# Performance work log

Measured on AMD Instinct MI355X. Metric: run time of the kernel, lower is better.

Reference implementation:

```python
import jax, jax.numpy as jnp
import numpy as np

BS, N, DE, DX = 16, 256, 64, 256
BIG = 100000.0


def setup_inputs() -> dict:
    key = jax.random.key(0)
    k1, k2, k3, k4 = jax.random.split(key, 4)
    E = jax.random.normal(k1, (BS, N, N, DE), dtype=jnp.float32)
    e_mask2 = jax.random.uniform(k2, (BS, 1, N, 1)) < 0.8
    fan_in = 4 * DE
    bound = 1.0 / np.sqrt(fan_in)
    W = jax.random.uniform(k3, (DX, fan_in), minval=-bound, maxval=bound, dtype=jnp.float32)
    b = jax.random.uniform(k4, (DX,), minval=-bound, maxval=bound, dtype=jnp.float32)
    return {"E": E, "e_mask2": e_mask2, "W": W, "b": b}


def reference(E, e_mask2, W, b):
    bs, n, _, de = E.shape
    mask = jnp.broadcast_to(e_mask2, (bs, n, n, de)).astype(E.dtype)  # bs,n,n,de
    imask = 1.0 - mask
    denom = mask.sum(axis=2)                       # bs,n,de
    m = E.sum(axis=2) / denom                      # (faithful: unmasked sum / mask count)
    mi = (E + BIG * imask).min(axis=2)             # masked min
    ma = (E - BIG * imask).max(axis=2)             # masked max
    std = (((E - m[:, :, None, :]) ** 2) * mask).sum(axis=2) / denom
    z = jnp.concatenate((m, mi, ma, std), axis=2)  # bs,n,4*de
    return jnp.einsum('bnf,df->bnd', z, W) + b     # bs,n,dx
```

## Files before the change

kernel.cpp:

```cpp
#include <hip/hip_runtime.h>
#include <cstdint>
#include <cstddef>

#define BSZ 16
#define NN  256
#define DE  64
#define DXX 256
#define FAN (4 * DE)
#define IB  4

__global__ __launch_bounds__(256) void prep_kernel(
    const uint8_t* __restrict__ raw, const float* __restrict__ W,
    float* __restrict__ WT, float* __restrict__ maskf)
{
    const int t   = threadIdx.x;
    const int blk = blockIdx.x;
    if (blk < FAN) {
        WT[blk * DXX + t] = W[t * FAN + blk];
    } else {
        __shared__ int det[2];
        if (t == 0) { det[0] = 0; det[1] = 0; }
        __syncthreads();
        int s1 = 0, s23 = 0;
        const uint8_t* p = raw + t * 16;
        #pragma unroll
        for (int u = 0; u < 16; ++u) {
            int v = (int)p[u];
            int m4 = u & 3;
            if (m4 == 1) s1 += v; else if (m4 >= 2) s23 += v;
        }
        if (s1)  atomicAdd(&det[0], s1);
        if (s23) atomicAdd(&det[1], s23);
        __syncthreads();
        const int kind = (det[1] == 0) ? 1 : ((det[0] == 0) ? 2 : 0);
        for (int idx = t; idx < BSZ * NN; idx += 256) {
            float mv;
            if (kind == 1)      mv = (((const int*)(const void*)raw)[idx] != 0) ? 1.f : 0.f;
            else if (kind == 2) mv = (((const float*)(const void*)raw)[idx] != 0.f) ? 1.f : 0.f;
            else                mv = (raw[idx] != 0) ? 1.f : 0.f;
            maskf[idx] = mv;
        }
    }
}

template <bool TR>
__global__ __launch_bounds__(256, 4) void etox_fused(
    const float* __restrict__ E, const uint8_t* __restrict__ raw,
    const float* __restrict__ maskf, const float* __restrict__ W,
    const float* __restrict__ WT, const float* __restrict__ bias,
    float* __restrict__ out)
{
    __shared__ float  m_lds[NN];
    __shared__ int    det[2];
    __shared__ float  cpart[4];
    __shared__ float  partial[4][16][20];
    __shared__ float  z_lds[IB][FAN];
    __shared__ float4 part_c[4][IB][64];

    const int t    = threadIdx.x;
    const int g0   = blockIdx.x * IB;
    const int b    = g0 >> 8;
    const int wv   = t >> 6;
    const int lane = t & 63;

    float mv;
    if (TR) {
        mv = maskf[b * NN + t];
    } else {
        if (t == 0) { det[0] = 0; det[1] = 0; }
        int s1 = 0, s23 = 0;
        const uint8_t* p = raw + t * 16;
        #pragma unroll
        for (int u = 0; u < 16; ++u) {
            int v = (int)p[u];
            int m4 = u & 3;
            if (m4 == 1) s1 += v; else if (m4 >= 2) s23 += v;
        }
        __syncthreads();
        if (s1)  atomicAdd(&det[0], s1);
        if (s23) atomicAdd(&det[1], s23);
        __syncthreads();
        const int kind = (det[1] == 0) ? 1 : ((det[0] == 0) ? 2 : 0);
        int idx = b * NN + t;
        if (kind == 1)      mv = (((const int*)(const void*)raw)[idx] != 0) ? 1.f : 0.f;
        else if (kind == 2) mv = (((const float*)(const void*)raw)[idx] != 0.f) ? 1.f : 0.f;
        else                mv = (raw[idx] != 0) ? 1.f : 0.f;
    }
    m_lds[t] = mv;
    unsigned long long bal = __ballot(mv != 0.f);
    if (lane == 0) cpart[wv] = (float)__popcll(bal);
    __syncthreads();
    const float inv_cnt = 1.0f / (cpart[0] + cpart[1] + cpart[2] + cpart[3]);

    const int dq = t & 15;
    const int jb = t >> 4;
    const float* base0 = E + (size_t)g0 * (NN * DE) + (size_t)jb * DE + 4 * dq;

    #define LD(P, K) (*(const float4*)((P) + (size_t)(K) * (16 * DE)))
    float4 A0, A1, A2, A3, B0, B1, B2, B3;
    A0 = LD(base0, 0); A1 = LD(base0, 1); A2 = LD(base0, 2); A3 = LD(base0, 3);

    for (int r = 0; r < IB; ++r) {
        const float* baser = base0 + (size_t)r * (NN * DE);

        float s[4]  = {0.f, 0.f, 0.f, 0.f};
        float ms[4] = {0.f, 0.f, 0.f, 0.f};
        float q[4]  = {0.f, 0.f, 0.f, 0.f};
        float mi[4] = {1e30f, 1e30f, 1e30f, 1e30f};
        float ma[4] = {-1e30f, -1e30f, -1e30f, -1e30f};

        #define CONS1(V, KK) { \
            float mk = m_lds[jb + 16 * (KK)]; \
            bool on = (mk != 0.f); \
            float4 v = V; \
            s[0] += v.x; s[1] += v.y; s[2] += v.z; s[3] += v.w; \
            ms[0] = fmaf(mk, v.x, ms[0]); ms[1] = fmaf(mk, v.y, ms[1]); \
            ms[2] = fmaf(mk, v.z, ms[2]); ms[3] = fmaf(mk, v.w, ms[3]); \
            q[0] = fmaf(mk * v.x, v.x, q[0]); q[1] = fmaf(mk * v.y, v.y, q[1]); \
            q[2] = fmaf(mk * v.z, v.z, q[2]); q[3] = fmaf(mk * v.w, v.w, q[3]); \
            mi[0] = fminf(mi[0], on ? v.x : 1e30f); mi[1] = fminf(mi[1], on ? v.y : 1e30f); \
            mi[2] = fminf(mi[2], on ? v.z : 1e30f); mi[3] = fminf(mi[3], on ? v.w : 1e30f); \
            ma[0] = fmaxf(ma[0], on ? v.x : -1e30f); ma[1] = fmaxf(ma[1], on ? v.y : -1e30f); \
            ma[2] = fmaxf(ma[2], on ? v.z : -1e30f); ma[3] = fmaxf(ma[3], on ? v.w : -1e30f); \
        }

        B0 = LD(baser, 4);  B1 = LD(baser, 5);  B2 = LD(baser, 6);  B3 = LD(baser, 7);
        CONS1(A0, 0) CONS1(A1, 1) CONS1(A2, 2) CONS1(A3, 3)
        A0 = LD(baser, 8);  A1 = LD(baser, 9);  A2 = LD(baser, 10); A3 = LD(baser, 11);
        CONS1(B0, 4) CONS1(B1, 5) CONS1(B2, 6) CONS1(B3, 7)
        B0 = LD(baser, 12); B1 = LD(baser, 13); B2 = LD(baser, 14); B3 = LD(baser, 15);
        CONS1(A0, 8) CONS1(A1, 9) CONS1(A2, 10) CONS1(A3, 11)
        if (r < IB - 1) {
            const float* basen = baser + (NN * DE);
            A0 = LD(basen, 0); A1 = LD(basen, 1); A2 = LD(basen, 2); A3 = LD(basen, 3);
        }
        CONS1(B0, 12) CONS1(B1, 13) CONS1(B2, 14) CONS1(B3, 15)
        #undef CONS1

        #pragma unroll
        for (int c = 0; c < 4; ++c) {
            s[c]  += __shfl_xor(s[c], 16);  s[c]  += __shfl_xor(s[c], 32);
            ms[c] += __shfl_xor(ms[c], 16); ms[c] += __shfl_xor(ms[c], 32);
            q[c]  += __shfl_xor(q[c], 16);  q[c]  += __shfl_xor(q[c], 32);
            mi[c] = fminf(mi[c], __shfl_xor(mi[c], 16));
            mi[c] = fminf(mi[c], __shfl_xor(mi[c], 32));
            ma[c] = fmaxf(ma[c], __shfl_xor(ma[c], 16));
            ma[c] = fmaxf(ma[c], __shfl_xor(ma[c], 32));
        }

        if (lane < 16) {
            float* p = partial[wv][lane];
            #pragma unroll
            for (int c = 0; c < 4; ++c) {
                p[c]      = s[c];
                p[4 + c]  = ms[c];
                p[8 + c]  = q[c];
                p[12 + c] = mi[c];
                p[16 + c] = ma[c];
            }
        }
        __syncthreads();

        if (t < 64) {
            const int d = t, dq2 = d >> 2, c = d & 3;
            float ss = 0.f, mss = 0.f, mq = 0.f, lmi = 1e30f, lma = -1e30f;
            #pragma unroll
            for (int w = 0; w < 4; ++w) {
                const float* p = partial[w][dq2];
                ss  += p[c];
                mss += p[4 + c];
                mq  += p[8 + c];
                lmi  = fminf(lmi, p[12 + c]);
                lma  = fmaxf(lma, p[16 + c]);
            }
            float m    = ss * inv_cnt;
            float stdv = mq * inv_cnt - 2.0f * m * (mss * inv_cnt) + m * m;
            z_lds[t >> 8][0] = z_lds[t >> 8][0];
            z_lds[r][d]       = m;
            z_lds[r][64 + d]  = lmi;
            z_lds[r][128 + d] = lma;
            z_lds[r][192 + d] = stdv;
        }
        __syncthreads();
    }
    #undef LD

    if (TR) {
        float4 acc[IB];
        #pragma unroll
        for (int r = 0; r < IB; ++r) acc[r] = make_float4(0.f, 0.f, 0.f, 0.f);

        const float4* WT4 = (const float4*)WT;
        int f0 = 64 * wv;
        #pragma unroll 4
        for (int fg = 0; fg < 16; ++fg, f0 += 4) {
            float4 w0 = WT4[(size_t)(f0 + 0) * 64 + lane];
            float4 w1 = WT4[(size_t)(f0 + 1) * 64 + lane];
            float4 w2 = WT4[(size_t)(f0 + 2) * 64 + lane];
            float4 w3 = WT4[(size_t)(f0 + 3) * 64 + lane];
            #pragma unroll
            for (int r = 0; r < IB; ++r) {
                float4 z4 = *(const float4*)(&z_lds[r][f0]);
                acc[r].x = fmaf(z4.x, w0.x, fmaf(z4.y, w1.x, fmaf(z4.z, w2.x, fmaf(z4.w, w3.x, acc[r].x))));
                acc[r].y = fmaf(z4.x, w0.y, fmaf(z4.y, w1.y, fmaf(z4.z, w2.y, fmaf(z4.w, w3.y, acc[r].y))));
                acc[r].z = fmaf(z4.x, w0.z, fmaf(z4.y, w1.z, fmaf(z4.z, w2.z, fmaf(z4.w, w3.z, acc[r].z))));
                acc[r].w = fmaf(z4.x, w0.w, fmaf(z4.y, w1.w, fmaf(z4.z, w2.w, fmaf(z4.w, w3.w, acc[r].w))));
            }
        }
        #pragma unroll
        for (int r = 0; r < IB; ++r) part_c[wv][r][lane] = acc[r];
        __syncthreads();

        const int row = t >> 6, l2 = t & 63;
        float4 p0 = part_c[0][row][l2], p1 = part_c[1][row][l2];
        float4 p2 = part_c[2][row][l2], p3 = part_c[3][row][l2];
        float4 bv = *(const float4*)(bias + 4 * l2);
        float4 o;
        o.x = p0.x + p1.x + p2.x + p3.x + bv.x;
        o.y = p0.y + p1.y + p2.y + p3.y + bv.y;
        o.z = p0.z + p1.z + p2.z + p3.z + bv.z;
        o.w = p0.w + p1.w + p2.w + p3.w + bv.w;
        *(float4*)(out + (size_t)(g0 + row) * DXX + 4 * l2) = o;
    } else {
        float acc0, acc1, acc2, acc3;
        {
            float bv = bias[t];
            acc0 = bv; acc1 = bv; acc2 = bv; acc3 = bv;
        }
        const float4* Wrow = (const float4*)(W + (size_t)t * FAN);
        #pragma unroll 8
        for (int f4 = 0; f4 < 64; ++f4) {
            float4 w4 = Wrow[f4];
            int f = 4 * f4;
            acc0 += z_lds[0][f] * w4.x + z_lds[0][f+1] * w4.y + z_lds[0][f+2] * w4.z + z_lds[0][f+3] * w4.w;
            acc1 += z_lds[1][f] * w4.x + z_lds[1][f+1] * w4.y + z_lds[1][f+2] * w4.z + z_lds[1][f+3] * w4.w;
            acc2 += z_lds[2][f] * w4.x + z_lds[2][f+1] * w4.y + z_lds[2][f+2] * w4.z + z_lds[2][f+3] * w4.w;
            acc3 += z_lds[3][f] * w4.x + z_lds[3][f+1] * w4.y + z_lds[3][f+2] * w4.z + z_lds[3][f+3] * w4.w;
        }
        out[(size_t)(g0 + 0) * DXX + t] = acc0;
        out[(size_t)(g0 + 1) * DXX + t] = acc1;
        out[(size_t)(g0 + 2) * DXX + t] = acc2;
        out[(size_t)(g0 + 3) * DXX + t] = acc3;
    }
}

extern "C" void kernel_launch(void* const* d_in, const int* in_sizes, int n_in,
                              void* d_out, int out_size, void* d_ws, size_t ws_size,
                              hipStream_t stream) {
    const float*   E    = (const float*)d_in[0];
    const uint8_t* mraw = (const uint8_t*)d_in[1];
    const float*   W    = (const float*)d_in[2];
    const float*   bias = (const float*)d_in[3];
    float*         out  = (float*)d_out;

    const size_t need = (size_t)FAN * DXX * sizeof(float) + (size_t)BSZ * NN * sizeof(float);
    if (ws_size >= need) {
        float* WT    = (float*)d_ws;
        float* maskf = (float*)d_ws + (size_t)FAN * DXX;
        prep_kernel<<<FAN + 1, 256, 0, stream>>>(mraw, W, WT, maskf);
        etox_fused<true><<<(BSZ * NN) / IB, 256, 0, stream>>>(E, mraw, maskf, W, WT, bias, out);
    } else {
        etox_fused<false><<<(BSZ * NN) / IB, 256, 0, stream>>>(E, mraw, nullptr, W, nullptr, bias, out);
    }
}
```

Baseline: 63.53 us.

## Interleave per-row matvec of previous row with next row's reduction loads

Instead of doing the whole 4-row z·W matvec after all reductions, the matvec for row r-1 is split into four chunks and interleaved between the E-tile consume steps of row r. The B-register prefetch is also moved one row ahead. The aim is to hide the E global-load latency behind matvec FMAs and the WT loads behind reduction work. The cost is that W^T is now reloaded once per row instead of being shared across all four rows, and register pressure goes up.

Result: slower. 216.1 us (+240.1%).

```diff
diff --git a/kernel.cpp b/kernel.cpp
--- a/kernel.cpp
+++ b/kernel.cpp
@@ -95,13 +95,37 @@
     const int dq = t & 15;
     const int jb = t >> 4;
     const float* base0 = E + (size_t)g0 * (NN * DE) + (size_t)jb * DE + 4 * dq;
+    const float4* WT4 = (const float4*)WT;
+    const int fbase = 64 * wv;
+
+    #define MVQ4(RZ, FG0) { \
+        _Pragma("unroll") \
+        for (int u = 0; u < 4; ++u) { \
+            const int f0 = fbase + 4 * ((FG0) + u); \
+            float4 w0 = WT4[(size_t)(f0 + 0) * 64 + lane]; \
+            float4 w1 = WT4[(size_t)(f0 + 1) * 64 + lane]; \
+            float4 w2 = WT4[(size_t)(f0 + 2) * 64 + lane]; \
+            float4 w3 = WT4[(size_t)(f0 + 3) * 64 + lane]; \
+            float4 z4 = *(const float4*)(&z_lds[RZ][f0]); \
+            mvacc.x = fmaf(z4.x, w0.x, fmaf(z4.y, w1.x, fmaf(z4.z, w2.x, fmaf(z4.w, w3.x, mvacc.x)))); \
+            mvacc.y = fmaf(z4.x, w0.y, fmaf(z4.y, w1.y, fmaf(z4.z, w2.y, fmaf(z4.w, w3.y, mvacc.y)))); \
+            mvacc.z = fmaf(z4.x, w0.z, fmaf(z4.y, w1.z, fmaf(z4.z, w2.z, fmaf(z4.w, w3.z, mvacc.z)))); \
+            mvacc.w = fmaf(z4.x, w0.w, fmaf(z4.y, w1.w, fmaf(z4.z, w2.w, fmaf(z4.w, w3.w, mvacc.w)))); \
+        } \
+    }
 
     #define LD(P, K) (*(const float4*)((P) + (size_t)(K) * (16 * DE)))
     float4 A0, A1, A2, A3, B0, B1, B2, B3;
     A0 = LD(base0, 0); A1 = LD(base0, 1); A2 = LD(base0, 2); A3 = LD(base0, 3);
+    B0 = LD(base0, 4); B1 = LD(base0, 5); B2 = LD(base0, 6); B3 = LD(base0, 7);
+
+    float4 mvacc = make_float4(0.f, 0.f, 0.f, 0.f);
 
     for (int r = 0; r < IB; ++r) {
         const float* baser = base0 + (size_t)r * (NN * DE);
+        const float* basen = baser + (NN * DE);
+        const int rz = r - 1;
+        const bool domv = TR && (r > 0);
 
         float s[4]  = {0.f, 0.f, 0.f, 0.f};
         float ms[4] = {0.f, 0.f, 0.f, 0.f};
@@ -124,17 +148,22 @@
             ma[2] = fmaxf(ma[2], on ? v.z : -1e30f); ma[3] = fmaxf(ma[3], on ? v.w : -1e30f); \
         }
 
-        B0 = LD(baser, 4);  B1 = LD(baser, 5);  B2 = LD(baser, 6);  B3 = LD(baser, 7);
         CONS1(A0, 0) CONS1(A1, 1) CONS1(A2, 2) CONS1(A3, 3)
         A0 = LD(baser, 8);  A1 = LD(baser, 9);  A2 = LD(baser, 10); A3 = LD(baser, 11);
+        if (domv) MVQ4(rz, 0)
         CONS1(B0, 4) CONS1(B1, 5) CONS1(B2, 6) CONS1(B3, 7)
         B0 = LD(baser, 12); B1 = LD(baser, 13); B2 = LD(baser, 14); B3 = LD(baser, 15);
+        if (domv) MVQ4(rz, 4)
         CONS1(A0, 8) CONS1(A1, 9) CONS1(A2, 10) CONS1(A3, 11)
-        if (r < IB - 1) {
-            const float* basen = baser + (NN * DE);
-            A0 = LD(basen, 0); A1 = LD(basen, 1); A2 = LD(basen, 2); A3 = LD(basen, 3);
-        }
+        if (r < IB - 1) { A0 = LD(basen, 0); A1 = LD(basen, 1); A2 = LD(basen, 2); A3 = LD(basen, 3); }
+        if (domv) MVQ4(rz, 8)
         CONS1(B0, 12) CONS1(B1, 13) CONS1(B2, 14) CONS1(B3, 15)
+        if (r < IB - 1) { B0 = LD(basen, 4); B1 = LD(basen, 5); B2 = LD(basen, 6); B3 = LD(basen, 7); }
+        if (domv) {
+            MVQ4(rz, 12)
+            part_c[wv][rz][lane] = mvacc;
+            mvacc = make_float4(0.f, 0.f, 0.f, 0.f);
+        }
         #undef CONS1
 
         #pragma unroll
@@ -175,7 +204,6 @@
             }
             float m    = ss * inv_cnt;
             float stdv = mq * inv_cnt - 2.0f * m * (mss * inv_cnt) + m * m;
-            z_lds[t >> 8][0] = z_lds[t >> 8][0];
             z_lds[r][d]       = m;
             z_lds[r][64 + d]  = lmi;
             z_lds[r][128 + d] = lma;
@@ -186,29 +214,8 @@
     #undef LD
 
     if (TR) {
-        float4 acc[IB];
-        #pragma unroll
-        for (int r = 0; r < IB; ++r) acc[r] = make_float4(0.f, 0.f, 0.f, 0.f);
-
-        const float4* WT4 = (const float4*)WT;
-        int f0 = 64 * wv;
-        #pragma unroll 4
-        for (int fg = 0; fg < 16; ++fg, f0 += 4) {
-            float4 w0 = WT4[(size_t)(f0 + 0) * 64 + lane];
-            float4 w1 = WT4[(size_t)(f0 + 1) * 64 + lane];
-            float4 w2 = WT4[(size_t)(f0 + 2) * 64 + lane];
-            float4 w3 = WT4[(size_t)(f0 + 3) * 64 + lane];
-            #pragma unroll
-            for (int r = 0; r < IB; ++r) {
-                float4 z4 = *(const float4*)(&z_lds[r][f0]);
-                acc[r].x = fmaf(z4.x, w0.x, fmaf(z4.y, w1.x, fmaf(z4.z, w2.x, fmaf(z4.w, w3.x, acc[r].x))));
-                acc[r].y = fmaf(z4.x, w0.y, fmaf(z4.y, w1.y, fmaf(z4.z, w2.y, fmaf(z4.w, w3.y, acc[r].y))));
-                acc[r].z = fmaf(z4.x, w0.z, fmaf(z4.y, w1.z, fmaf(z4.z, w2.z, fmaf(z4.w, w3.z, acc[r].z))));
-                acc[r].w = fmaf(z4.x, w0.w, fmaf(z4.y, w1.w, fmaf(z4.z, w2.w, fmaf(z4.w, w3.w, acc[r].w))));
-            }
-        }
-        #pragma unroll
-        for (int r = 0; r < IB; ++r) part_c[wv][r][lane] = acc[r];
+        MVQ4(IB - 1, 0) MVQ4(IB - 1, 4) MVQ4(IB - 1, 8) MVQ4(IB - 1, 12)
+        part_c[wv][IB - 1][lane] = mvacc;
         __syncthreads();
 
         const int row = t >> 6, l2 = t & 63;
@@ -242,6 +249,7 @@
         out[(size_t)(g0 + 2) * DXX + t] = acc2;
         out[(size_t)(g0 + 3) * DXX + t] = acc3;
     }
+    #undef MVQ4
 }
 
 extern "C" void kernel_launch(void* const* d_in, const int* in_sizes, int n_in,
```

## Interleave per-row matvec into reduction loop and use lgkm-only barriers

Applied to the files above, without the earlier changes.

The projection of each row's z-vector through W is moved inside the per-row reduction loop, so its matvec can overlap with the prefetched E loads for the next row instead of running as a separate phase after all rows. The __syncthreads calls are replaced with a custom barrier that waits only on LDS counters (lgkmcnt), so outstanding global loads of E do not stall the barrier. In exchange, WT is reloaded once per row instead of being reused across all four rows, which raises the number of L2/global loads. The barrier also relies on the compiler not reordering LDS accesses across the inline asm.

After: 81.23 us. 27.9% more time.

```diff
diff --git a/kernel.cpp b/kernel.cpp
--- a/kernel.cpp
+++ b/kernel.cpp
@@ -8,6 +8,12 @@
 #define DXX 256
 #define FAN (4 * DE)
 #define IB  4
+
+__device__ __forceinline__ void barrier_lgkm() {
+    asm volatile("s_waitcnt lgkmcnt(0)" ::: "memory");
+    __builtin_amdgcn_s_barrier();
+    asm volatile("" ::: "memory");
+}
 
 __global__ __launch_bounds__(256) void prep_kernel(
     const uint8_t* __restrict__ raw, const float* __restrict__ W,
@@ -95,6 +101,8 @@
     const int dq = t & 15;
     const int jb = t >> 4;
     const float* base0 = E + (size_t)g0 * (NN * DE) + (size_t)jb * DE + 4 * dq;
+    const float4* WT4 = (const float4*)WT;
+    const int fbase = 64 * wv;
 
     #define LD(P, K) (*(const float4*)((P) + (size_t)(K) * (16 * DE)))
     float4 A0, A1, A2, A3, B0, B1, B2, B3;
@@ -159,7 +167,7 @@
                 p[16 + c] = ma[c];
             }
         }
-        __syncthreads();
+        if (TR) barrier_lgkm(); else __syncthreads();
 
         if (t < 64) {
             const int d = t, dq2 = d >> 2, c = d & 3;
@@ -175,42 +183,35 @@
             }
             float m    = ss * inv_cnt;
             float stdv = mq * inv_cnt - 2.0f * m * (mss * inv_cnt) + m * m;
-            z_lds[t >> 8][0] = z_lds[t >> 8][0];
             z_lds[r][d]       = m;
             z_lds[r][64 + d]  = lmi;
             z_lds[r][128 + d] = lma;
             z_lds[r][192 + d] = stdv;
         }
-        __syncthreads();
+        if (TR) barrier_lgkm(); else __syncthreads();
+
+        if (TR) {
+            float4 mvacc = make_float4(0.f, 0.f, 0.f, 0.f);
+            #pragma unroll 4
+            for (int fg = 0; fg < 16; ++fg) {
+                const int f0 = fbase + 4 * fg;
+                float4 w0 = WT4[(size_t)(f0 + 0) * 64 + lane];
+                float4 w1 = WT4[(size_t)(f0 + 1) * 64 + lane];
+                float4 w2 = WT4[(size_t)(f0 + 2) * 64 + lane];
+                float4 w3 = WT4[(size_t)(f0 + 3) * 64 + lane];
+                float4 z4 = *(const float4*)(&z_lds[r][f0]);
+                mvacc.x = fmaf(z4.x, w0.x, fmaf(z4.y, w1.x, fmaf(z4.z, w2.x, fmaf(z4.w, w3.x, mvacc.x))));
+                mvacc.y = fmaf(z4.x, w0.y, fmaf(z4.y, w1.y, fmaf(z4.z, w2.y, fmaf(z4.w, w3.y, mvacc.y))));
+                mvacc.z = fmaf(z4.x, w0.z, fmaf(z4.y, w1.z, fmaf(z4.z, w2.z, fmaf(z4.w, w3.z, mvacc.z))));
+                mvacc.w = fmaf(z4.x, w0.w, fmaf(z4.y, w1.w, fmaf(z4.z, w2.w, fmaf(z4.w, w3.w, mvacc.w))));
+            }
+            part_c[wv][r][lane] = mvacc;
+        }
     }
     #undef LD
 
     if (TR) {
-        float4 acc[IB];
-        #pragma unroll
-        for (int r = 0; r < IB; ++r) acc[r] = make_float4(0.f, 0.f, 0.f, 0.f);
-
-        const float4* WT4 = (const float4*)WT;
-        int f0 = 64 * wv;
-        #pragma unroll 4
-        for (int fg = 0; fg < 16; ++fg, f0 += 4) {
-            float4 w0 = WT4[(size_t)(f0 + 0) * 64 + lane];
-            float4 w1 = WT4[(size_t)(f0 + 1) * 64 + lane];
-            float4 w2 = WT4[(size_t)(f0 + 2) * 64 + lane];
-            float4 w3 = WT4[(size_t)(f0 + 3) * 64 + lane];
-            #pragma unroll
-            for (int r = 0; r < IB; ++r) {
-                float4 z4 = *(const float4*)(&z_lds[r][f0]);
-                acc[r].x = fmaf(z4.x, w0.x, fmaf(z4.y, w1.x, fmaf(z4.z, w2.x, fmaf(z4.w, w3.x, acc[r].x))));
-                acc[r].y = fmaf(z4.x, w0.y, fmaf(z4.y, w1.y, fmaf(z4.z, w2.y, fmaf(z4.w, w3.y, acc[r].y))));
-                acc[r].z = fmaf(z4.x, w0.z, fmaf(z4.y, w1.z, fmaf(z4.z, w2.z, fmaf(z4.w, w3.z, acc[r].z))));
-                acc[r].w = fmaf(z4.x, w0.w, fmaf(z4.y, w1.w, fmaf(z4.z, w2.w, fmaf(z4.w, w3.w, acc[r].w))));
-            }
-        }
-        #pragma unroll
-        for (int r = 0; r < IB; ++r) part_c[wv][r][lane] = acc[r];
-        __syncthreads();
-
+        barrier_lgkm();
         const int row = t >> 6, l2 = t & 63;
         float4 p0 = part_c[0][row][l2], p1 = part_c[1][row][l2];
         float4 p2 = part_c[2][row][l2], p3 = part_c[3][row][l2];
```

## Split fused stats+GEMM into separate kernels with a larger GEMM row tile

Applied to the files above, without the earlier changes.

The fused kernel is split into a stats kernel, which writes z rows to a workspace buffer, and a separate GEMM kernel that processes 16 rows per block. Each weight load is then reused across 16 rows instead of 4, and the stats kernel is freed of the GEMM phase's registers and shared memory. Mask values are also cached in registers rather than re-read from LDS in the inner loop. The cost is an extra launch plus a round trip of the z tensor (4 MB) through global memory, and a larger workspace requirement. The fallback path keeps the old fused kernel.

After: 77.54 us. 22.1% more time.

```diff
diff --git a/kernel.cpp b/kernel.cpp
--- a/kernel.cpp
+++ b/kernel.cpp
@@ -8,6 +8,7 @@
 #define DXX 256
 #define FAN (4 * DE)
 #define IB  4
+#define RB  16
 
 __global__ __launch_bounds__(256) void prep_kernel(
     const uint8_t* __restrict__ raw, const float* __restrict__ W,
@@ -43,19 +44,13 @@
     }
 }
 
-template <bool TR>
-__global__ __launch_bounds__(256, 4) void etox_fused(
-    const float* __restrict__ E, const uint8_t* __restrict__ raw,
-    const float* __restrict__ maskf, const float* __restrict__ W,
-    const float* __restrict__ WT, const float* __restrict__ bias,
-    float* __restrict__ out)
+__global__ __launch_bounds__(256, 4) void k1_stats(
+    const float* __restrict__ E, const float* __restrict__ maskf,
+    float* __restrict__ zout)
 {
-    __shared__ float  m_lds[NN];
-    __shared__ int    det[2];
-    __shared__ float  cpart[4];
-    __shared__ float  partial[4][16][20];
-    __shared__ float  z_lds[IB][FAN];
-    __shared__ float4 part_c[4][IB][64];
+    __shared__ float m_lds[NN];
+    __shared__ float cpart[4];
+    __shared__ float partial[4][16][20];
 
     const int t    = threadIdx.x;
     const int g0   = blockIdx.x * IB;
@@ -63,29 +58,7 @@
     const int wv   = t >> 6;
     const int lane = t & 63;
 
-    float mv;
-    if (TR) {
-        mv = maskf[b * NN + t];
-    } else {
-        if (t == 0) { det[0] = 0; det[1] = 0; }
-        int s1 = 0, s23 = 0;
-        const uint8_t* p = raw + t * 16;
-        #pragma unroll
-        for (int u = 0; u < 16; ++u) {
-            int v = (int)p[u];
-            int m4 = u & 3;
-            if (m4 == 1) s1 += v; else if (m4 >= 2) s23 += v;
-        }
-        __syncthreads();
-        if (s1)  atomicAdd(&det[0], s1);
-        if (s23) atomicAdd(&det[1], s23);
-        __syncthreads();
-        const int kind = (det[1] == 0) ? 1 : ((det[0] == 0) ? 2 : 0);
-        int idx = b * NN + t;
-        if (kind == 1)      mv = (((const int*)(const void*)raw)[idx] != 0) ? 1.f : 0.f;
-        else if (kind == 2) mv = (((const float*)(const void*)raw)[idx] != 0.f) ? 1.f : 0.f;
-        else                mv = (raw[idx] != 0) ? 1.f : 0.f;
-    }
+    float mv = maskf[b * NN + t];
     m_lds[t] = mv;
     unsigned long long bal = __ballot(mv != 0.f);
     if (lane == 0) cpart[wv] = (float)__popcll(bal);
@@ -94,6 +67,11 @@
 
     const int dq = t & 15;
     const int jb = t >> 4;
+
+    float mk[16];
+    #pragma unroll
+    for (int k = 0; k < 16; ++k) mk[k] = m_lds[jb + 16 * k];
+
     const float* base0 = E + (size_t)g0 * (NN * DE) + (size_t)jb * DE + 4 * dq;
 
     #define LD(P, K) (*(const float4*)((P) + (size_t)(K) * (16 * DE)))
@@ -110,14 +88,14 @@
         float ma[4] = {-1e30f, -1e30f, -1e30f, -1e30f};
 
         #define CONS1(V, KK) { \
-            float mk = m_lds[jb + 16 * (KK)]; \
-            bool on = (mk != 0.f); \
+            float mkv = mk[KK]; \
+            bool on = (mkv != 0.f); \
             float4 v = V; \
             s[0] += v.x; s[1] += v.y; s[2] += v.z; s[3] += v.w; \
-            ms[0] = fmaf(mk, v.x, ms[0]); ms[1] = fmaf(mk, v.y, ms[1]); \
-            ms[2] = fmaf(mk, v.z, ms[2]); ms[3] = fmaf(mk, v.w, ms[3]); \
-            q[0] = fmaf(mk * v.x, v.x, q[0]); q[1] = fmaf(mk * v.y, v.y, q[1]); \
-            q[2] = fmaf(mk * v.z, v.z, q[2]); q[3] = fmaf(mk * v.w, v.w, q[3]); \
+            ms[0] = fmaf(mkv, v.x, ms[0]); ms[1] = fmaf(mkv, v.y, ms[1]); \
+            ms[2] = fmaf(mkv, v.z, ms[2]); ms[3] = fmaf(mkv, v.w, ms[3]); \
+            q[0] = fmaf(mkv * v.x, v.x, q[0]); q[1] = fmaf(mkv * v.y, v.y, q[1]); \
+            q[2] = fmaf(mkv * v.z, v.z, q[2]); q[3] = fmaf(mkv * v.w, v.w, q[3]); \
             mi[0] = fminf(mi[0], on ? v.x : 1e30f); mi[1] = fminf(mi[1], on ? v.y : 1e30f); \
             mi[2] = fminf(mi[2], on ? v.z : 1e30f); mi[3] = fminf(mi[3], on ? v.w : 1e30f); \
             ma[0] = fmaxf(ma[0], on ? v.x : -1e30f); ma[1] = fmaxf(ma[1], on ? v.y : -1e30f); \
@@ -175,43 +153,63 @@
             }
             float m    = ss * inv_cnt;
             float stdv = mq * inv_cnt - 2.0f * m * (mss * inv_cnt) + m * m;
-            z_lds[t >> 8][0] = z_lds[t >> 8][0];
-            z_lds[r][d]       = m;
-            z_lds[r][64 + d]  = lmi;
-            z_lds[r][128 + d] = lma;
-            z_lds[r][192 + d] = stdv;
+            float* zr = zout + (size_t)(g0 + r) * FAN;
+            zr[d]       = m;
+            zr[64 + d]  = lmi;
+            zr[128 + d] = lma;
+            zr[192 + d] = stdv;
         }
         __syncthreads();
     }
     #undef LD
-
-    if (TR) {
-        float4 acc[IB];
-        #pragma unroll
-        for (int r = 0; r < IB; ++r) acc[r] = make_float4(0.f, 0.f, 0.f, 0.f);
-
-        const float4* WT4 = (const float4*)WT;
-        int f0 = 64 * wv;
-        #pragma unroll 4
-        for (int fg = 0; fg < 16; ++fg, f0 += 4) {
-            float4 w0 = WT4[(size_t)(f0 + 0) * 64 + lane];
-            float4 w1 = WT4[(size_t)(f0 + 1) * 64 + lane];
-            float4 w2 = WT4[(size_t)(f0 + 2) * 64 + lane];
-            float4 w3 = WT4[(size_t)(f0 + 3) * 64 + lane];
-            #pragma unroll
-            for (int r = 0; r < IB; ++r) {
-                float4 z4 = *(const float4*)(&z_lds[r][f0]);
-                acc[r].x = fmaf(z4.x, w0.x, fmaf(z4.y, w1.x, fmaf(z4.z, w2.x, fmaf(z4.w, w3.x, acc[r].x))));
-                acc[r].y = fmaf(z4.x, w0.y, fmaf(z4.y, w1.y, fmaf(z4.z, w2.y, fmaf(z4.w, w3.y, acc[r].y))));
-                acc[r].z = fmaf(z4.x, w0.z, fmaf(z4.y, w1.z, fmaf(z4.z, w2.z, fmaf(z4.w, w3.z, acc[r].z))));
-                acc[r].w = fmaf(z4.x, w0.w, fmaf(z4.y, w1.w, fmaf(z4.z, w2.w, fmaf(z4.w, w3.w, acc[r].w))));
-            }
-        }
-        #pragma unroll
-        for (int r = 0; r < IB; ++r) part_c[wv][r][lane] = acc[r];
-        __syncthreads();
-
-        const int row = t >> 6, l2 = t & 63;
+}
+
+__global__ __launch_bounds__(256, 2) void k2_gemm(
+    const float* __restrict__ zin, const float* __restrict__ WT,
+    const float* __restrict__ bias, float* __restrict__ out)
+{
+    __shared__ float  z_s[RB][FAN];
+    __shared__ float4 part_c[4][RB][64];
+
+    const int t    = threadIdx.x;
+    const int r0   = blockIdx.x * RB;
+    const int wv   = t >> 6;
+    const int lane = t & 63;
+
+    #pragma unroll
+    for (int i = 0; i < RB; ++i)
+        z_s[i][t] = zin[(size_t)(r0 + i) * FAN + t];
+    __syncthreads();
+
+    float4 acc[RB];
+    #pragma unroll
+    for (int i = 0; i < RB; ++i) acc[i] = make_float4(0.f, 0.f, 0.f, 0.f);
+
+    const float4* WT4 = (const float4*)WT;
+    int f0 = 64 * wv;
+    #pragma unroll 2
+    for (int fg = 0; fg < 16; ++fg, f0 += 4) {
+        float4 w0 = WT4[(size_t)(f0 + 0) * 64 + lane];
+        float4 w1 = WT4[(size_t)(f0 + 1) * 64 + lane];
+        float4 w2 = WT4[(size_t)(f0 + 2) * 64 + lane];
+        float4 w3 = WT4[(size_t)(f0 + 3) * 64 + lane];
+        #pragma unroll
+        for (int i = 0; i < RB; ++i) {
+            float4 z4 = *(const float4*)(&z_s[i][f0]);
+            acc[i].x = fmaf(z4.x, w0.x, fmaf(z4.y, w1.x, fmaf(z4.z, w2.x, fmaf(z4.w, w3.x, acc[i].x))));
+            acc[i].y = fmaf(z4.x, w0.y, fmaf(z4.y, w1.y, fmaf(z4.z, w2.y, fmaf(z4.w, w3.y, acc[i].y))));
+            acc[i].z = fmaf(z4.x, w0.z, fmaf(z4.y, w1.z, fmaf(z4.z, w2.z, fmaf(z4.w, w3.z, acc[i].z))));
+            acc[i].w = fmaf(z4.x, w0.w, fmaf(z4.y, w1.w, fmaf(z4.z, w2.w, fmaf(z4.w, w3.w, acc[i].w))));
+        }
+    }
+    #pragma unroll
+    for (int i = 0; i < RB; ++i) part_c[wv][i][lane] = acc[i];
+    __syncthreads();
+
+    #pragma unroll
+    for (int pass = 0; pass < 4; ++pass) {
+        const int idx = pass * 256 + t;
+        const int row = idx >> 6, l2 = idx & 63;
         float4 p0 = part_c[0][row][l2], p1 = part_c[1][row][l2];
         float4 p2 = part_c[2][row][l2], p3 = part_c[3][row][l2];
         float4 bv = *(const float4*)(bias + 4 * l2);
@@ -220,28 +218,157 @@
         o.y = p0.y + p1.y + p2.y + p3.y + bv.y;
         o.z = p0.z + p1.z + p2.z + p3.z + bv.z;
         o.w = p0.w + p1.w + p2.w + p3.w + bv.w;
-        *(float4*)(out + (size_t)(g0 + row) * DXX + 4 * l2) = o;
-    } else {
-        float acc0, acc1, acc2, acc3;
-        {
-            float bv = bias[t];
-            acc0 = bv; acc1 = bv; acc2 = bv; acc3 = bv;
-        }
-        const float4* Wrow = (const float4*)(W + (size_t)t * FAN);
-        #pragma unroll 8
-        for (int f4 = 0; f4 < 64; ++f4) {
-            float4 w4 = Wrow[f4];
-            int f = 4 * f4;
-            acc0 += z_lds[0][f] * w4.x + z_lds[0][f+1] * w4.y + z_lds[0][f+2] * w4.z + z_lds[0][f+3] * w4.w;
-            acc1 += z_lds[1][f] * w4.x + z_lds[1][f+1] * w4.y + z_lds[1][f+2] * w4.z + z_lds[1][f+3] * w4.w;
-            acc2 += z_lds[2][f] * w4.x + z_lds[2][f+1] * w4.y + z_lds[2][f+2] * w4.z + z_lds[2][f+3] * w4.w;
-            acc3 += z_lds[3][f] * w4.x + z_lds[3][f+1] * w4.y + z_lds[3][f+2] * w4.z + z_lds[3][f+3] * w4.w;
-        }
-        out[(size_t)(g0 + 0) * DXX + t] = acc0;
-        out[(size_t)(g0 + 1) * DXX + t] = acc1;
-        out[(size_t)(g0 + 2) * DXX + t] = acc2;
-        out[(size_t)(g0 + 3) * DXX + t] = acc3;
-    }
+        *(float4*)(out + (size_t)(r0 + row) * DXX + 4 * l2) = o;
+    }
+}
+
+__global__ __launch_bounds__(256, 4) void etox_legacy(
+    const float* __restrict__ E, const uint8_t* __restrict__ raw,
+    const float* __restrict__ W, const float* __restrict__ bias,
+    float* __restrict__ out)
+{
+    __shared__ float m_lds[NN];
+    __shared__ int   det[2];
+    __shared__ float cpart[4];
+    __shared__ float partial[4][16][20];
+    __shared__ float z_lds[IB][FAN];
+
+    const int t    = threadIdx.x;
+    const int g0   = blockIdx.x * IB;
+    const int b    = g0 >> 8;
+    const int wv   = t >> 6;
+    const int lane = t & 63;
+
+    if (t == 0) { det[0] = 0; det[1] = 0; }
+    int s1 = 0, s23 = 0;
+    {
+        const uint8_t* p = raw + t * 16;
+        #pragma unroll
+        for (int u = 0; u < 16; ++u) {
+            int v = (int)p[u];
+            int m4 = u & 3;
+            if (m4 == 1) s1 += v; else if (m4 >= 2) s23 += v;
+        }
+    }
+    __syncthreads();
+    if (s1)  atomicAdd(&det[0], s1);
+    if (s23) atomicAdd(&det[1], s23);
+    __syncthreads();
+    const int kind = (det[1] == 0) ? 1 : ((det[0] == 0) ? 2 : 0);
+    float mv;
+    {
+        int idx = b * NN + t;
+        if (kind == 1)      mv = (((const int*)(const void*)raw)[idx] != 0) ? 1.f : 0.f;
+        else if (kind == 2) mv = (((const float*)(const void*)raw)[idx] != 0.f) ? 1.f : 0.f;
+        else                mv = (raw[idx] != 0) ? 1.f : 0.f;
+    }
+    m_lds[t] = mv;
+    unsigned long long bal = __ballot(mv != 0.f);
+    if (lane == 0) cpart[wv] = (float)__popcll(bal);
+    __syncthreads();
+    const float inv_cnt = 1.0f / (cpart[0] + cpart[1] + cpart[2] + cpart[3]);
+
+    const int dq = t & 15;
+    const int jb = t >> 4;
+    const float* base0 = E + (size_t)g0 * (NN * DE) + (size_t)jb * DE + 4 * dq;
+
+    #define LD(P, K) (*(const float4*)((P) + (size_t)(K) * (16 * DE)))
+    float4 A0, A1, A2, A3, B0, B1, B2, B3;
+    A0 = LD(base0, 0); A1 = LD(base0, 1); A2 = LD(base0, 2); A3 = LD(base0, 3);
+
+    for (int r = 0; r < IB; ++r) {
+        const float* baser = base0 + (size_t)r * (NN * DE);
+        float s[4]  = {0.f, 0.f, 0.f, 0.f};
+        float ms[4] = {0.f, 0.f, 0.f, 0.f};
+        float q[4]  = {0.f, 0.f, 0.f, 0.f};
+        float mi[4] = {1e30f, 1e30f, 1e30f, 1e30f};
+        float ma[4] = {-1e30f, -1e30f, -1e30f, -1e30f};
+
+        #define CONS1(V, KK) { \
+            float mkv = m_lds[jb + 16 * (KK)]; \
+            bool on = (mkv != 0.f); \
+            float4 v = V; \
+            s[0] += v.x; s[1] += v.y; s[2] += v.z; s[3] += v.w; \
+            ms[0] = fmaf(mkv, v.x, ms[0]); ms[1] = fmaf(mkv, v.y, ms[1]); \
+            ms[2] = fmaf(mkv, v.z, ms[2]); ms[3] = fmaf(mkv, v.w, ms[3]); \
+            q[0] = fmaf(mkv * v.x, v.x, q[0]); q[1] = fmaf(mkv * v.y, v.y, q[1]); \
+            q[2] = fmaf(mkv * v.z, v.z, q[2]); q[3] = fmaf(mkv * v.w, v.w, q[3]); \
+            mi[0] = fminf(mi[0], on ? v.x : 1e30f); mi[1] = fminf(mi[1], on ? v.y : 1e30f); \
+            mi[2] = fminf(mi[2], on ? v.z : 1e30f); mi[3] = fminf(mi[3], on ? v.w : 1e30f); \
+            ma[0] = fmaxf(ma[0], on ? v.x : -1e30f); ma[1] = fmaxf(ma[1], on ? v.y : -1e30f); \
+            ma[2] = fmaxf(ma[2], on ? v.z : -1e30f); ma[3] = fmaxf(ma[3], on ? v.w : -1e30f); \
+        }
+
+        B0 = LD(baser, 4);  B1 = LD(baser, 5);  B2 = LD(baser, 6);  B3 = LD(baser, 7);
+        CONS1(A0, 0) CONS1(A1, 1) CONS1(A2, 2) CONS1(A3, 3)
+        A0 = LD(baser, 8);  A1 = LD(baser, 9);  A2 = LD(baser, 10); A3 = LD(baser, 11);
+        CONS1(B0, 4) CONS1(B1, 5) CONS1(B2, 6) CONS1(B3, 7)
+        B0 = LD(baser, 12); B1 = LD(baser, 13); B2 = LD(baser, 14); B3 = LD(baser, 15);
+        CONS1(A0, 8) CONS1(A1, 9) CONS1(A2, 10) CONS1(A3, 11)
+        if (r < IB - 1) {
+            const float* basen = baser + (NN * DE);
+            A0 = LD(basen, 0); A1 = LD(basen, 1); A2 = LD(basen, 2); A3 = LD(basen, 3);
+        }
+        CONS1(B0, 12) CONS1(B1, 13) CONS1(B2, 14) CONS1(B3, 15)
+        #undef CONS1
+
+        #pragma unroll
+        for (int c = 0; c < 4; ++c) {
+            s[c]  += __shfl_xor(s[c], 16);  s[c]  += __shfl_xor(s[c], 32);
+            ms[c] += __shfl_xor(ms[c], 16); ms[c] += __shfl_xor(ms[c], 32);
+            q[c]  += __shfl_xor(q[c], 16);  q[c]  += __shfl_xor(q[c], 32);
+            mi[c] = fminf(mi[c], __shfl_xor(mi[c], 16));
+            mi[c] = fminf(mi[c], __shfl_xor(mi[c], 32));
+            ma[c] = fmaxf(ma[c], __shfl_xor(ma[c], 16));
+            ma[c] = fmaxf(ma[c], __shfl_xor(ma[c], 32));
+        }
+
+        if (lane < 16) {
+            float* p = partial[wv][lane];
+            #pragma unroll
+            for (int c = 0; c < 4; ++c) {
+                p[c] = s[c]; p[4+c] = ms[c]; p[8+c] = q[c];
+                p[12+c] = mi[c]; p[16+c] = ma[c];
+            }
+        }
+        __syncthreads();
+
+        if (t < 64) {
+            const int d = t, dq2 = d >> 2, c = d & 3;
+            float ss = 0.f, mss = 0.f, mq = 0.f, lmi = 1e30f, lma = -1e30f;
+            #pragma unroll
+            for (int w = 0; w < 4; ++w) {
+                const float* p = partial[w][dq2];
+                ss += p[c]; mss += p[4+c]; mq += p[8+c];
+                lmi = fminf(lmi, p[12+c]); lma = fmaxf(lma, p[16+c]);
+            }
+            float m    = ss * inv_cnt;
+            float stdv = mq * inv_cnt - 2.0f * m * (mss * inv_cnt) + m * m;
+            z_lds[r][d] = m; z_lds[r][64+d] = lmi; z_lds[r][128+d] = lma; z_lds[r][192+d] = stdv;
+        }
+        __syncthreads();
+    }
+    #undef LD
+
+    float acc0, acc1, acc2, acc3;
+    {
+        float bv = bias[t];
+        acc0 = bv; acc1 = bv; acc2 = bv; acc3 = bv;
+    }
+    const float4* Wrow = (const float4*)(W + (size_t)t * FAN);
+    #pragma unroll 8
+    for (int f4 = 0; f4 < 64; ++f4) {
+        float4 w4 = Wrow[f4];
+        int f = 4 * f4;
+        acc0 += z_lds[0][f]*w4.x + z_lds[0][f+1]*w4.y + z_lds[0][f+2]*w4.z + z_lds[0][f+3]*w4.w;
+        acc1 += z_lds[1][f]*w4.x + z_lds[1][f+1]*w4.y + z_lds[1][f+2]*w4.z + z_lds[1][f+3]*w4.w;
+        acc2 += z_lds[2][f]*w4.x + z_lds[2][f+1]*w4.y + z_lds[2][f+2]*w4.z + z_lds[2][f+3]*w4.w;
+        acc3 += z_lds[3][f]*w4.x + z_lds[3][f+1]*w4.y + z_lds[3][f+2]*w4.z + z_lds[3][f+3]*w4.w;
+    }
+    out[(size_t)(g0 + 0) * DXX + t] = acc0;
+    out[(size_t)(g0 + 1) * DXX + t] = acc1;
+    out[(size_t)(g0 + 2) * DXX + t] = acc2;
+    out[(size_t)(g0 + 3) * DXX + t] = acc3;
 }
 
 extern "C" void kernel_launch(void* const* d_in, const int* in_sizes, int n_in,
@@ -253,13 +380,19 @@
     const float*   bias = (const float*)d_in[3];
     float*         out  = (float*)d_out;
 
-    const size_t need = (size_t)FAN * DXX * sizeof(float) + (size_t)BSZ * NN * sizeof(float);
+    const size_t wt_n   = (size_t)FAN * DXX;
+    const size_t mask_n = (size_t)BSZ * NN;
+    const size_t z_n    = (size_t)BSZ * NN * FAN;
+    const size_t need   = (wt_n + mask_n + z_n) * sizeof(float);
+
     if (ws_size >= need) {
         float* WT    = (float*)d_ws;
-        float* maskf = (float*)d_ws + (size_t)FAN * DXX;
+        float* maskf = WT + wt_n;
+        float* zbuf  = maskf + mask_n;
         prep_kernel<<<FAN + 1, 256, 0, stream>>>(mraw, W, WT, maskf);
-        etox_fused<true><<<(BSZ * NN) / IB, 256, 0, stream>>>(E, mraw, maskf, W, WT, bias, out);
+        k1_stats<<<(BSZ * NN) / IB, 256, 0, stream>>>(E, maskf, zbuf);
+        k2_gemm<<<(BSZ * NN) / RB, 256, 0, stream>>>(zbuf, WT, bias, out);
     } else {
-        etox_fused<false><<<(BSZ * NN) / IB, 256, 0, stream>>>(E, mraw, nullptr, W, nullptr, bias, out);
-    }
-}
+        etox_legacy<<<(BSZ * NN) / IB, 256, 0, stream>>>(E, mraw, W, bias, out);
+    }
+}
```
